# Kernel optimization log

Measured on AMD Instinct MI355X. Metric: run time of the kernel, lower is better.

The kernel has to match this reference:

```python
import jax, jax.numpy as jnp
import numpy as np

OUTPUT_DIM = 572
D_MODEL = 1024  # 256 * network_scale^2, network_scale=2
BATCH = 16384


def setup_inputs() -> dict:
    key = jax.random.key(0)
    k1, k2, k3 = jax.random.split(key, 3)
    core_output = jax.random.normal(k1, (BATCH, D_MODEL), dtype=jnp.float32)
    W1 = jax.random.normal(k2, (D_MODEL, OUTPUT_DIM), dtype=jnp.float32) * 0.02
    b1 = jnp.zeros((OUTPUT_DIM,), dtype=jnp.float32)
    W2 = jax.random.normal(k3, (OUTPUT_DIM, D_MODEL), dtype=jnp.float32) * 0.02
    b2 = jnp.zeros((D_MODEL,), dtype=jnp.float32)
    return {"core_output": core_output, "W1": W1, "b1": b1, "W2": W2, "b2": b2}


def reference(core_output, W1, b1, W2, b2):
    # Dense -> Softmax (note: the original returns softmax probs under the name
    # 'action_type_logits')
    pre = core_output @ W1 + b1                       # [B, O]
    probs = jax.nn.softmax(pre, axis=-1)              # [B, O]
    # Categorical(probs).sample() == gumbel-argmax over log-probs
    log_probs = jax.nn.log_softmax(pre, axis=-1)
    action_type = jax.random.categorical(jax.random.key(42), log_probs, axis=-1)  # [B] int32
    # one_hot(action_type) @ W2 is a row gather from W2
    hidden = W2[action_type] + b2                     # [B, D]
    autoregressive_embedding = jax.nn.relu(hidden) + core_output  # residual add
    return probs, autoregressive_embedding
```

## Files before the change

### kernel.cpp

```cpp
#include <hip/hip_runtime.h>
#include <hip/hip_fp16.h>
#include <stdint.h>

#define M_TOTAL 16384
#define N_TOTAL 572
#define N_PAD   640
#define K_TOTAL 1024
#define D_TOTAL 1024

typedef _Float16 f16;
typedef __attribute__((ext_vector_type(8))) _Float16 f16x8;
typedef __attribute__((ext_vector_type(4))) float f32x4;

__global__ __launch_bounds__(256) void convert_w(const float* __restrict__ W,
                                                 f16* __restrict__ thi,
                                                 f16* __restrict__ tlo) {
  __shared__ float tile[32][33];
  const int n0 = blockIdx.x * 32, k0 = blockIdx.y * 32;
  const int tx = threadIdx.x & 31, ty = threadIdx.x >> 5;
#pragma unroll
  for (int s = 0; s < 32; s += 8) {
    const int k = k0 + ty + s, n = n0 + tx;
    tile[ty + s][tx] = (n < N_TOTAL) ? W[(size_t)k * N_TOTAL + n] : 0.0f;
  }
  __syncthreads();
#pragma unroll
  for (int s = 0; s < 32; s += 8) {
    const int n = n0 + ty + s, k = k0 + tx;
    const float x = tile[tx][ty + s];
    const f16 h = (f16)x;
    thi[(size_t)n * K_TOTAL + k] = h;
    tlo[(size_t)n * K_TOTAL + k] = (f16)(x - (float)h);
  }
}

#define BM 128
#define BN 128
#define BK 32
#define LDK 40

__global__ __launch_bounds__(256) void gemm_fused(
    const float* __restrict__ A,
    const f16* __restrict__ bHi, const f16* __restrict__ bLo,
    const float* __restrict__ b1, float* __restrict__ C) {
  __shared__ __align__(16) f16 As[2][BM][LDK];
  __shared__ __align__(16) f16 Bs[2][BN][LDK];

  const int t = threadIdx.x;
  const int lane = t & 63, wid = t >> 6;
  const int wm = wid >> 1, wn = wid & 1;

  const int bid = blockIdx.x;
  const int wg = (bid & 7) * 80 + (bid >> 3);
  const int nb = wg % 5, mb = wg / 5;
  const int m0 = mb * BM, n0 = nb * BN;

  const int r0 = t >> 1, hf = t & 1;

  f32x4 acc[2][4] = {};
  float4 pa[4];
  f16x8 pbh[2], pbl[2];

  const float* aBase = A + (size_t)(m0 + r0) * K_TOTAL + hf * 16;
  const f16* bhBase = bHi + (size_t)(n0 + r0) * K_TOTAL + hf * 16;
  const f16* blBase = bLo + (size_t)(n0 + r0) * K_TOTAL + hf * 16;

  auto LOADK = [&](int k0) {
#pragma unroll
    for (int i = 0; i < 4; ++i)
      pa[i] = *reinterpret_cast<const float4*>(aBase + k0 + i * 4);
#pragma unroll
    for (int i = 0; i < 2; ++i) {
      pbh[i] = *reinterpret_cast<const f16x8*>(bhBase + k0 + i * 8);
      pbl[i] = *reinterpret_cast<const f16x8*>(blBase + k0 + i * 8);
    }
  };
  auto WRITELDS = [&]() {
    const float x[16] = {pa[0].x, pa[0].y, pa[0].z, pa[0].w,
                         pa[1].x, pa[1].y, pa[1].z, pa[1].w,
                         pa[2].x, pa[2].y, pa[2].z, pa[2].w,
                         pa[3].x, pa[3].y, pa[3].z, pa[3].w};
    f16x8 vh[2], vl[2];
#pragma unroll
    for (int e = 0; e < 16; ++e) {
      const f16 h = (f16)x[e];
      vh[e >> 3][e & 7] = h;
      vl[e >> 3][e & 7] = (f16)(x[e] - (float)h);
    }
#pragma unroll
    for (int i = 0; i < 2; ++i) {
      *reinterpret_cast<f16x8*>(&As[0][r0][hf * 16 + i * 8]) = vh[i];
      *reinterpret_cast<f16x8*>(&As[1][r0][hf * 16 + i * 8]) = vl[i];
      *reinterpret_cast<f16x8*>(&Bs[0][r0][hf * 16 + i * 8]) = pbh[i];
      *reinterpret_cast<f16x8*>(&Bs[1][r0][hf * 16 + i * 8]) = pbl[i];
    }
  };

  const int fr = lane & 15, fq = lane >> 4;

  LOADK(0);
  for (int k0 = 0; k0 < K_TOTAL; k0 += BK) {
    __syncthreads();
    WRITELDS();
    if (k0 + BK < K_TOTAL) LOADK(k0 + BK);
    __syncthreads();

    f16x8 ah[2], al[2];
#pragma unroll
    for (int mi = 0; mi < 2; ++mi) {
      const int row = wm * 32 + mi * 16 + fr;
      ah[mi] = *reinterpret_cast<const f16x8*>(&As[0][row][fq * 8]);
      al[mi] = *reinterpret_cast<const f16x8*>(&As[1][row][fq * 8]);
    }
#pragma unroll
    for (int ni = 0; ni < 4; ++ni) {
      const int row = wn * 64 + ni * 16 + fr;
      const f16x8 bh = *reinterpret_cast<const f16x8*>(&Bs[0][row][fq * 8]);
      const f16x8 bl = *reinterpret_cast<const f16x8*>(&Bs[1][row][fq * 8]);
#pragma unroll
      for (int mi = 0; mi < 2; ++mi) {
        acc[mi][ni] = __builtin_amdgcn_mfma_f32_16x16x32_f16(ah[mi], bh, acc[mi][ni], 0, 0, 0);
        acc[mi][ni] = __builtin_amdgcn_mfma_f32_16x16x32_f16(ah[mi], bl, acc[mi][ni], 0, 0, 0);
        acc[mi][ni] = __builtin_amdgcn_mfma_f32_16x16x32_f16(al[mi], bh, acc[mi][ni], 0, 0, 0);
      }
    }
  }

#pragma unroll
  for (int ni = 0; ni < 4; ++ni) {
    const int n = n0 + wn * 64 + ni * 16 + fr;
    if (n >= N_TOTAL) continue;
    const float bb = b1[n];
#pragma unroll
    for (int mi = 0; mi < 2; ++mi) {
      const int mbase = m0 + wm * 32 + mi * 16 + fq * 4;
#pragma unroll
      for (int r = 0; r < 4; ++r)
        C[(size_t)(mbase + r) * N_TOTAL + n] = acc[mi][ni][r] + bb;
    }
  }
}

__global__ __launch_bounds__(256) void gemm_pre(const float* __restrict__ A,
                                                const float* __restrict__ W,
                                                const float* __restrict__ b1,
                                                float* __restrict__ C) {
  __shared__ float As_[16][64];
  __shared__ float Bs_[16][64];
  const int t = threadIdx.x;
  const int tx = t & 15, ty = t >> 4;
  const int m0 = blockIdx.y * 64;
  const int n0 = blockIdx.x * 64;
  const int ar = t >> 2, ac4 = (t & 3) << 2;
  const int bk = t >> 4, bn4 = (t & 15) << 2;
  float acc[4][4] = {};
  for (int k0 = 0; k0 < K_TOTAL; k0 += 16) {
    float4 av = *reinterpret_cast<const float4*>(A + (size_t)(m0 + ar) * K_TOTAL + k0 + ac4);
    As_[ac4 + 0][ar] = av.x;
    As_[ac4 + 1][ar] = av.y;
    As_[ac4 + 2][ar] = av.z;
    As_[ac4 + 3][ar] = av.w;
    float4 bv = make_float4(0.f, 0.f, 0.f, 0.f);
    const int gn = n0 + bn4;
    if (gn < N_TOTAL)
      bv = *reinterpret_cast<const float4*>(W + (size_t)(k0 + bk) * N_TOTAL + gn);
    *reinterpret_cast<float4*>(&Bs_[bk][bn4]) = bv;
    __syncthreads();
#pragma unroll
    for (int kk = 0; kk < 16; ++kk) {
      float4 a = *reinterpret_cast<const float4*>(&As_[kk][ty << 2]);
      float4 b = *reinterpret_cast<const float4*>(&Bs_[kk][tx << 2]);
      const float aa[4] = {a.x, a.y, a.z, a.w};
      const float bb[4] = {b.x, b.y, b.z, b.w};
#pragma unroll
      for (int i = 0; i < 4; ++i)
#pragma unroll
        for (int j = 0; j < 4; ++j)
          acc[i][j] = fmaf(aa[i], bb[j], acc[i][j]);
    }
    __syncthreads();
  }
#pragma unroll
  for (int j = 0; j < 4; ++j) {
    const int n = n0 + (tx << 2) + j;
    if (n < N_TOTAL) {
      const float bj = b1[n];
#pragma unroll
      for (int i = 0; i < 4; ++i) {
        const int m = m0 + (ty << 2) + i;
        C[(size_t)m * N_TOTAL + n] = acc[i][j] + bj;
      }
    }
  }
}

__device__ __forceinline__ float jax_gumbel(uint32_t idx) {
  const uint32_t ks0 = 0u;
  const uint32_t ks1 = 42u;
  const uint32_t ks2 = 0x1BD11BDAu ^ ks0 ^ ks1;
  uint32_t x0 = ks0;
  uint32_t x1 = idx + ks1;
#define TF_ROUND(r) { x0 += x1; x1 = (x1 << (r)) | (x1 >> (32 - (r))); x1 ^= x0; }
  TF_ROUND(13) TF_ROUND(15) TF_ROUND(26) TF_ROUND(6)
  x0 += ks1; x1 += ks2 + 1u;
  TF_ROUND(17) TF_ROUND(29) TF_ROUND(16) TF_ROUND(24)
  x0 += ks2; x1 += ks0 + 2u;
  TF_ROUND(13) TF_ROUND(15) TF_ROUND(26) TF_ROUND(6)
  x0 += ks0; x1 += ks1 + 3u;
  TF_ROUND(17) TF_ROUND(29) TF_ROUND(16) TF_ROUND(24)
  x0 += ks1; x1 += ks2 + 4u;
  TF_ROUND(13) TF_ROUND(15) TF_ROUND(26) TF_ROUND(6)
  x0 += ks2; x1 += ks0 + 5u;
#undef TF_ROUND
  const uint32_t bits = x0 ^ x1;
  union { uint32_t u; float f; } cvt;
  cvt.u = (bits >> 9) | 0x3F800000u;
  const float fl = cvt.f - 1.0f;
  const float TINY = 1.1754943508222875e-38f;
  const float u = fmaxf(TINY, fl * 1.0f + TINY);
  return -logf(-logf(u));
}

__global__ __launch_bounds__(256) void head_kernel(
    float* __restrict__ pre_probs,
    const float* __restrict__ core,
    const float* __restrict__ W2,
    const float* __restrict__ b2,
    float* __restrict__ out1) {
  const int row = blockIdx.x;
  const int t = threadIdx.x;
  const int lane = t & 63, wid = t >> 6;

  __shared__ float s_max[4];
  __shared__ float s_sum[4];
  __shared__ float s_av[4];
  __shared__ int   s_ai[4];

  float* xrow = pre_probs + (size_t)row * N_TOTAL;
  const int c0 = t, c1 = t + 256, c2 = t + 512;
  const bool v1 = (c1 < N_TOTAL), v2 = (c2 < N_TOTAL);
  const float NEG_INF = -__builtin_inff();

  const float x0v = xrow[c0];
  const float x1v = v1 ? xrow[c1] : NEG_INF;
  const float x2v = v2 ? xrow[c2] : NEG_INF;

  float vmax = fmaxf(x0v, fmaxf(x1v, x2v));
#pragma unroll
  for (int off = 32; off > 0; off >>= 1)
    vmax = fmaxf(vmax, __shfl_xor(vmax, off, 64));
  if (lane == 0) s_max[wid] = vmax;
  __syncthreads();
  const float m = fmaxf(fmaxf(s_max[0], s_max[1]), fmaxf(s_max[2], s_max[3]));

  const float e0 = expf(x0v - m);
  const float e1 = v1 ? expf(x1v - m) : 0.0f;
  const float e2 = v2 ? expf(x2v - m) : 0.0f;
  float vsum = e0 + e1 + e2;
#pragma unroll
  for (int off = 32; off > 0; off >>= 1)
    vsum += __shfl_xor(vsum, off, 64);
  if (lane == 0) s_sum[wid] = vsum;
  __syncthreads();
  const float sum = (s_sum[0] + s_sum[1]) + (s_sum[2] + s_sum[3]);

  const float lse = logf(sum);
  xrow[c0] = e0 / sum;
  if (v1) xrow[c1] = e1 / sum;
  if (v2) xrow[c2] = e2 / sum;

  const uint32_t base = (uint32_t)row * (uint32_t)N_TOTAL;
  float bv = jax_gumbel(base + c0) + ((x0v - m) - lse);
  int bi = c0;
  if (v1) {
    const float s1 = jax_gumbel(base + c1) + ((x1v - m) - lse);
    if (s1 > bv) { bv = s1; bi = c1; }
  }
  if (v2) {
    const float s2 = jax_gumbel(base + c2) + ((x2v - m) - lse);
    if (s2 > bv) { bv = s2; bi = c2; }
  }
#pragma unroll
  for (int off = 32; off > 0; off >>= 1) {
    const float ov = __shfl_xor(bv, off, 64);
    const int oi = __shfl_xor(bi, off, 64);
    if (ov > bv || (ov == bv && oi < bi)) { bv = ov; bi = oi; }
  }
  if (lane == 0) { s_av[wid] = bv; s_ai[wid] = bi; }
  __syncthreads();
  float best = s_av[0]; int action = s_ai[0];
#pragma unroll
  for (int w = 1; w < 4; ++w) {
    if (s_av[w] > best || (s_av[w] == best && s_ai[w] < action)) {
      best = s_av[w]; action = s_ai[w];
    }
  }

  const float* __restrict__ w2row = W2 + (size_t)action * D_TOTAL;
  const float* __restrict__ crow = core + (size_t)row * D_TOTAL;
  float* __restrict__ orow = out1 + (size_t)row * D_TOTAL;
#pragma unroll
  for (int d = t; d < D_TOTAL; d += 256) {
    const float h = w2row[d] + b2[d];
    orow[d] = fmaxf(h, 0.0f) + crow[d];
  }
}

extern "C" void kernel_launch(void* const* d_in, const int* in_sizes, int n_in,
                              void* d_out, int out_size, void* d_ws, size_t ws_size,
                              hipStream_t stream) {
  const float* core = (const float*)d_in[0];
  const float* W1   = (const float*)d_in[1];
  const float* b1   = (const float*)d_in[2];
  const float* W2   = (const float*)d_in[3];
  const float* b2   = (const float*)d_in[4];

  float* probs = (float*)d_out;
  float* out1  = (float*)d_out + (size_t)M_TOTAL * N_TOTAL;

  const size_t wneed = (size_t)2 * N_PAD * K_TOTAL * sizeof(f16);
  if (ws_size >= wneed) {
    f16* wHi = (f16*)d_ws;
    f16* wLo = wHi + (size_t)N_PAD * K_TOTAL;
    convert_w<<<dim3(N_PAD / 32, K_TOTAL / 32), 256, 0, stream>>>(W1, wHi, wLo);
    gemm_fused<<<(M_TOTAL / BM) * (N_PAD / BN), 256, 0, stream>>>(core, wHi, wLo, b1, probs);
  } else {
    gemm_pre<<<dim3((N_TOTAL + 63) / 64, M_TOTAL / 64), 256, 0, stream>>>(core, W1, b1, probs);
  }

  head_kernel<<<M_TOTAL, 256, 0, stream>>>(probs, core, W2, b2, out1);
}
```

Measured before the change: 122.8 us.

## Replace LDS-staged split-fp16 GEMM with direct global-to-register MFMA loads

Removes the shared-memory double-buffered staging of A and the hi/lo W1 tiles. Each wave now loads its A rows straight from global memory, splits them into fp16 hi/lo in registers, and loads B fragments from global memory, computing a 64x64 sub-tile with a 4x4 accumulator array. The aim is to drop the LDS writes and reads and the two barriers per K step. The trade-off is that tiles are no longer shared across waves, so each A and B element is re-fetched by more waves and the loads are less coalesced. The change also makes the waves cover all 128 rows of each block tile, which the previous mapping left half unwritten, so the amount of MFMA work per block doubles.

```diff
diff --git a/kernel.cpp b/kernel.cpp
--- a/kernel.cpp
+++ b/kernel.cpp
@@ -34,18 +34,10 @@
   }
 }
 
-#define BM 128
-#define BN 128
-#define BK 32
-#define LDK 40
-
-__global__ __launch_bounds__(256) void gemm_fused(
+__global__ __launch_bounds__(256) void gemm_direct(
     const float* __restrict__ A,
     const f16* __restrict__ bHi, const f16* __restrict__ bLo,
     const float* __restrict__ b1, float* __restrict__ C) {
-  __shared__ __align__(16) f16 As[2][BM][LDK];
-  __shared__ __align__(16) f16 Bs[2][BN][LDK];
-
   const int t = threadIdx.x;
   const int lane = t & 63, wid = t >> 6;
   const int wm = wid >> 1, wn = wid & 1;
@@ -53,72 +45,38 @@
   const int bid = blockIdx.x;
   const int wg = (bid & 7) * 80 + (bid >> 3);
   const int nb = wg % 5, mb = wg / 5;
-  const int m0 = mb * BM, n0 = nb * BN;
-
-  const int r0 = t >> 1, hf = t & 1;
-
-  f32x4 acc[2][4] = {};
-  float4 pa[4];
-  f16x8 pbh[2], pbl[2];
-
-  const float* aBase = A + (size_t)(m0 + r0) * K_TOTAL + hf * 16;
-  const f16* bhBase = bHi + (size_t)(n0 + r0) * K_TOTAL + hf * 16;
-  const f16* blBase = bLo + (size_t)(n0 + r0) * K_TOTAL + hf * 16;
-
-  auto LOADK = [&](int k0) {
-#pragma unroll
-    for (int i = 0; i < 4; ++i)
-      pa[i] = *reinterpret_cast<const float4*>(aBase + k0 + i * 4);
-#pragma unroll
-    for (int i = 0; i < 2; ++i) {
-      pbh[i] = *reinterpret_cast<const f16x8*>(bhBase + k0 + i * 8);
-      pbl[i] = *reinterpret_cast<const f16x8*>(blBase + k0 + i * 8);
-    }
-  };
-  auto WRITELDS = [&]() {
-    const float x[16] = {pa[0].x, pa[0].y, pa[0].z, pa[0].w,
-                         pa[1].x, pa[1].y, pa[1].z, pa[1].w,
-                         pa[2].x, pa[2].y, pa[2].z, pa[2].w,
-                         pa[3].x, pa[3].y, pa[3].z, pa[3].w};
-    f16x8 vh[2], vl[2];
-#pragma unroll
-    for (int e = 0; e < 16; ++e) {
-      const f16 h = (f16)x[e];
-      vh[e >> 3][e & 7] = h;
-      vl[e >> 3][e & 7] = (f16)(x[e] - (float)h);
-    }
-#pragma unroll
-    for (int i = 0; i < 2; ++i) {
-      *reinterpret_cast<f16x8*>(&As[0][r0][hf * 16 + i * 8]) = vh[i];
-      *reinterpret_cast<f16x8*>(&As[1][r0][hf * 16 + i * 8]) = vl[i];
-      *reinterpret_cast<f16x8*>(&Bs[0][r0][hf * 16 + i * 8]) = pbh[i];
-      *reinterpret_cast<f16x8*>(&Bs[1][r0][hf * 16 + i * 8]) = pbl[i];
-    }
-  };
+  const int m0 = mb * 128 + wm * 64;
+  const int n0 = nb * 128 + wn * 64;
 
   const int fr = lane & 15, fq = lane >> 4;
 
-  LOADK(0);
-  for (int k0 = 0; k0 < K_TOTAL; k0 += BK) {
-    __syncthreads();
-    WRITELDS();
-    if (k0 + BK < K_TOTAL) LOADK(k0 + BK);
-    __syncthreads();
-
-    f16x8 ah[2], al[2];
-#pragma unroll
-    for (int mi = 0; mi < 2; ++mi) {
-      const int row = wm * 32 + mi * 16 + fr;
-      ah[mi] = *reinterpret_cast<const f16x8*>(&As[0][row][fq * 8]);
-      al[mi] = *reinterpret_cast<const f16x8*>(&As[1][row][fq * 8]);
+  const float* aRow = A + (size_t)(m0 + fr) * K_TOTAL + fq * 8;
+  const f16* bhRow = bHi + (size_t)(n0 + fr) * K_TOTAL + fq * 8;
+  const f16* blRow = bLo + (size_t)(n0 + fr) * K_TOTAL + fq * 8;
+
+  f32x4 acc[4][4] = {};
+
+  for (int k0 = 0; k0 < K_TOTAL; k0 += 32) {
+    f16x8 ah[4], al[4];
+#pragma unroll
+    for (int mi = 0; mi < 4; ++mi) {
+      const float* p = aRow + (size_t)mi * 16 * K_TOTAL + k0;
+      const float4 v0 = *reinterpret_cast<const float4*>(p);
+      const float4 v1 = *reinterpret_cast<const float4*>(p + 4);
+      const float x[8] = {v0.x, v0.y, v0.z, v0.w, v1.x, v1.y, v1.z, v1.w};
+#pragma unroll
+      for (int j = 0; j < 8; ++j) {
+        const f16 h = (f16)x[j];
+        ah[mi][j] = h;
+        al[mi][j] = (f16)(x[j] - (float)h);
+      }
     }
 #pragma unroll
     for (int ni = 0; ni < 4; ++ni) {
-      const int row = wn * 64 + ni * 16 + fr;
-      const f16x8 bh = *reinterpret_cast<const f16x8*>(&Bs[0][row][fq * 8]);
-      const f16x8 bl = *reinterpret_cast<const f16x8*>(&Bs[1][row][fq * 8]);
-#pragma unroll
-      for (int mi = 0; mi < 2; ++mi) {
+      const f16x8 bh = *reinterpret_cast<const f16x8*>(bhRow + (size_t)ni * 16 * K_TOTAL + k0);
+      const f16x8 bl = *reinterpret_cast<const f16x8*>(blRow + (size_t)ni * 16 * K_TOTAL + k0);
+#pragma unroll
+      for (int mi = 0; mi < 4; ++mi) {
         acc[mi][ni] = __builtin_amdgcn_mfma_f32_16x16x32_f16(ah[mi], bh, acc[mi][ni], 0, 0, 0);
         acc[mi][ni] = __builtin_amdgcn_mfma_f32_16x16x32_f16(ah[mi], bl, acc[mi][ni], 0, 0, 0);
         acc[mi][ni] = __builtin_amdgcn_mfma_f32_16x16x32_f16(al[mi], bh, acc[mi][ni], 0, 0, 0);
@@ -128,12 +86,12 @@
 
 #pragma unroll
   for (int ni = 0; ni < 4; ++ni) {
-    const int n = n0 + wn * 64 + ni * 16 + fr;
+    const int n = n0 + ni * 16 + fr;
     if (n >= N_TOTAL) continue;
     const float bb = b1[n];
 #pragma unroll
-    for (int mi = 0; mi < 2; ++mi) {
-      const int mbase = m0 + wm * 32 + mi * 16 + fq * 4;
+    for (int mi = 0; mi < 4; ++mi) {
+      const int mbase = m0 + mi * 16 + fq * 4;
 #pragma unroll
       for (int r = 0; r < 4; ++r)
         C[(size_t)(mbase + r) * N_TOTAL + n] = acc[mi][ni][r] + bb;
@@ -323,7 +281,7 @@
     f16* wHi = (f16*)d_ws;
     f16* wLo = wHi + (size_t)N_PAD * K_TOTAL;
     convert_w<<<dim3(N_PAD / 32, K_TOTAL / 32), 256, 0, stream>>>(W1, wHi, wLo);
-    gemm_fused<<<(M_TOTAL / BM) * (N_PAD / BN), 256, 0, stream>>>(core, wHi, wLo, b1, probs);
+    gemm_direct<<<(M_TOTAL / 128) * (N_PAD / 128), 256, 0, stream>>>(core, wHi, wLo, b1, probs);
   } else {
     gemm_pre<<<dim3((N_TOTAL + 63) / 64, M_TOTAL / 64), 256, 0, stream>>>(core, W1, b1, probs);
   }
```

New measurement: 230.3 us. 1.88x slower.
